# Performance work log

Measured on AMD Instinct MI355X. Metric: run time of the kernel, lower is better.

## Reference

```python
import math
import jax, jax.numpy as jnp
import numpy as np

WQ = (24, 24)  # query window size
WK = (12, 12)  # key window size
NH = 8         # heads
D = 256        # d_model


def _ln(x, g, b, eps=1e-5):
    m = x.mean(-1, keepdims=True)
    v = ((x - m) ** 2).mean(-1, keepdims=True)
    return (x - m) / jnp.sqrt(v + eps) * g + b


def _sine_pos(F, Hp, Wp):
    # Faithful to PositionEmbeddingSine(normalize=True) applied to an NHWC tensor:
    # dim F (grid height) plays the role of channels; returns (F, Hp, Wp).
    npf = F // 2
    scale = 2.0 * math.pi
    eps = 1e-5
    y = jnp.arange(1, Hp + 1, dtype=jnp.float32) / (Hp + eps) * scale
    x = jnp.arange(1, Wp + 1, dtype=jnp.float32) / (Wp + eps) * scale
    dim_t = 10000.0 ** (2.0 * (jnp.arange(npf) // 2).astype(jnp.float32) / npf)
    def enc(e):
        p = e[:, None] / dim_t
        return jnp.stack([jnp.sin(p[:, 0::2]), jnp.cos(p[:, 1::2])], axis=2).reshape(e.shape[0], npf)
    py = enc(y)  # (Hp, npf)
    px = enc(x)  # (Wp, npf)
    pos = jnp.concatenate([
        jnp.broadcast_to(py[:, None, :], (Hp, Wp, npf)),
        jnp.broadcast_to(px[None, :, :], (Hp, Wp, npf))], axis=-1)
    return pos.transpose(2, 0, 1)


def _interp_ac(x, Ho, Wo):
    # bilinear, align_corners=True; x: (B, C, H, W)
    B, C, H, W = x.shape
    ys = jnp.linspace(0.0, H - 1.0, Ho)
    xs = jnp.linspace(0.0, W - 1.0, Wo)
    y0 = jnp.floor(ys).astype(jnp.int32); y1 = jnp.minimum(y0 + 1, H - 1); wy = ys - y0
    x0 = jnp.floor(xs).astype(jnp.int32); x1 = jnp.minimum(x0 + 1, W - 1); wx = xs - x0
    rows = x[:, :, y0, :] * (1 - wy)[None, None, :, None] + x[:, :, y1, :] * wy[None, None, :, None]
    return rows[:, :, :, x0] * (1 - wx) + rows[:, :, :, x1] * wx


def _wpart(x, wh, ww):
    B, H, W, C = x.shape
    return x.reshape(B, H // wh, wh, W // ww, ww, C).transpose(0, 1, 3, 2, 4, 5).reshape(-1, wh * ww, C)


def _avgpool(x, wh, ww):
    B, H, W, C = x.shape
    return x.reshape(B, H // wh, wh, W // ww, ww, C).mean(axis=(2, 4))


def _forward(x1, x2, q_w, q_b, k_w, k_b, v_w, v_b, q2_w, q2_b, k2_w, k2_b, v2_w, v2_b,
             proj_w, proj_b, proj_g, proj_beta, n1_g, n1_b, n2_g, n2_b,
             fc1_w, fc1_b, fc2_w, fc2_b):
    B, C1, H1, W1 = x1.shape
    _, C2, H2, W2 = x2.shape
    hd = D // NH
    x1n = x1.transpose(0, 2, 3, 1)
    sc = _ln(x1n @ proj_w + proj_b, proj_g, proj_beta)
    sc = _interp_ac(sc.transpose(0, 3, 1, 2), H2, W2).transpose(0, 2, 3, 1)
    x1p = jnp.pad(x1n, ((0, 0), (0, (-H1) % WK[0]), (0, (-W1) % WK[1]), (0, 0)))
    x2n = x2.transpose(0, 2, 3, 1)
    x2p = jnp.pad(x2n, ((0, 0), (0, (-H2) % WQ[0]), (0, (-W2) % WQ[1]), (0, 0)))
    H2p, W2p = x2p.shape[1], x2p.shape[2]
    qw = _wpart(x2p, *WQ)  # (B*nw, 576, C2)
    kw = _wpart(x1p, *WK)  # (B*nw, 144, C1)
    Bn, N1, _ = qw.shape
    def heads(t):
        return t.reshape(t.shape[0], t.shape[1], NH, hd).transpose(0, 2, 1, 3)
    q = heads(qw @ q_w + q_b)
    k = heads(kw @ k_w + k_b)
    v = heads(kw @ v_w + v_b)
    # NOTE: faithful to the source: scale = head_dim**(-0.0) == 1.0 and NO softmax here
    attn = q @ k.transpose(0, 1, 3, 2)
    o = (attn @ v).transpose(0, 2, 1, 3).reshape(Bn, N1, D)
    nwh, nww = H2p // WQ[0], W2p // WQ[1]
    o = o.reshape(B, nwh, nww, WQ[0], WQ[1], D).transpose(0, 1, 3, 2, 4, 5).reshape(B, H2p, W2p, D)
    qf = x2p + o
    # global (pooled) cross-attention branch
    qg = _avgpool(x2p, *WQ)
    qg = qg + _sine_pos(qg.shape[1], qg.shape[2], qg.shape[3])[None]
    kg = _avgpool(x1p, *WK)
    kg = kg + _sine_pos(kg.shape[1], kg.shape[2], kg.shape[3])[None]
    qg = qg.reshape(B, -1, C2)
    kg = kg.reshape(B, -1, C1)
    Nw = qg.shape[1]
    qg2 = heads(qg @ q2_w + q2_b)
    kg2 = heads(kg @ k2_w + k2_b)
    vg = heads(kg @ v2_w + v2_b)
    a2 = jax.nn.softmax(qg2 @ kg2.transpose(0, 1, 3, 2), axis=-1)
    og = (a2 @ vg).transpose(0, 2, 1, 3).reshape(B, Nw, D)
    og = og.transpose(0, 2, 1).reshape(B, D, nwh, nww)
    og = _interp_ac(og, H2p, W2p).transpose(0, 2, 3, 1)
    qf = (qf + og)[:, :H2, :W2, :]
    h = _ln(qf, n1_g, n1_b)
    h = jax.nn.gelu(h @ fc1_w + fc1_b, approximate=False) @ fc2_w + fc2_b
    out = sc + h
    return _ln(out, n2_g, n2_b).transpose(0, 3, 1, 2)


def setup_inputs() -> dict:
    key = jax.random.key(0)
    ks = jax.random.split(key, 12)
    B, C1, C2 = 2, 512, 256
    H1, W1, H2, W2 = 96, 96, 192, 192
    s = 0.02
    def lin(k, i, o):
        return jax.random.normal(k, (i, o), jnp.float32) * s
    return {
        'x1': jax.random.normal(ks[0], (B, C1, H1, W1), jnp.float32),
        'x2': jax.random.normal(ks[1], (B, C2, H2, W2), jnp.float32),
        'q_w': lin(ks[2], C2, D), 'q_b': jnp.zeros((D,), jnp.float32),
        'k_w': lin(ks[3], C1, D), 'k_b': jnp.zeros((D,), jnp.float32),
        'v_w': lin(ks[4], C1, D), 'v_b': jnp.zeros((D,), jnp.float32),
        'q2_w': lin(ks[5], C2, D), 'q2_b': jnp.zeros((D,), jnp.float32),
        'k2_w': lin(ks[6], C1, D), 'k2_b': jnp.zeros((D,), jnp.float32),
        'v2_w': lin(ks[7], C1, D), 'v2_b': jnp.zeros((D,), jnp.float32),
        'proj_w': lin(ks[8], C1, D), 'proj_b': jnp.zeros((D,), jnp.float32),
        'proj_g': jnp.ones((D,), jnp.float32), 'proj_beta': jnp.zeros((D,), jnp.float32),
        'n1_g': jnp.ones((D,), jnp.float32), 'n1_b': jnp.zeros((D,), jnp.float32),
        'n2_g': jnp.ones((D,), jnp.float32), 'n2_b': jnp.zeros((D,), jnp.float32),
        'fc1_w': lin(ks[9], D, 2 * D), 'fc1_b': jnp.zeros((2 * D,), jnp.float32),
        'fc2_w': lin(ks[10], 2 * D, D), 'fc2_b': jnp.zeros((D,), jnp.float32),
    }


def reference(x1, x2, q_w, q_b, k_w, k_b, v_w, v_b, q2_w, q2_b, k2_w, k2_b, v2_w, v2_b,
              proj_w, proj_b, proj_g, proj_beta, n1_g, n1_b, n2_g, n2_b,
              fc1_w, fc1_b, fc2_w, fc2_b):
    return _forward(x1, x2, q_w, q_b, k_w, k_b, v_w, v_b, q2_w, q2_b, k2_w, k2_b, v2_w, v2_b,
                    proj_w, proj_b, proj_g, proj_beta, n1_g, n1_b, n2_g, n2_b,
                    fc1_w, fc1_b, fc2_w, fc2_b)
```

## Files before the change

kernel.cpp:

```cpp
#include <hip/hip_runtime.h>
#include <math.h>


#define HW1 9216L
#define HW2 36864L
#define M1  18432L
#define M2  73728L

typedef __attribute__((ext_vector_type(8))) short short8;
typedef __attribute__((ext_vector_type(4))) float f32x4;
typedef unsigned short u16;

__device__ __forceinline__ short f2bf(float f)
{
    unsigned u = __builtin_bit_cast(unsigned, f);
    u = (u + 0x7fff + ((u >> 16) & 1)) >> 16;
    return (short)u;
}
__device__ __forceinline__ float bf2f(u16 u)
{
    unsigned x = ((unsigned)u) << 16;
    return __builtin_bit_cast(float, x);
}
__device__ __forceinline__ float gelu_exact(float v)
{
    return 0.5f * v * (1.0f + erff(v * 0.70710678118654752f));
}

__global__ __launch_bounds__(256) void wcvt(
    const float* __restrict__ pw, const float* __restrict__ kw,
    const float* __restrict__ vw, const float* __restrict__ qw,
    const float* __restrict__ f1, const float* __restrict__ f2,
    u16* __restrict__ pwT, u16* __restrict__ kwT, u16* __restrict__ vwT,
    u16* __restrict__ qwT, u16* __restrict__ f1T, u16* __restrict__ f2T)
{
    int bx = blockIdx.x, t = threadIdx.x;
    const float* src; u16* dst; int K, ldN = 256, kt, n0 = 0;
    if (bx < 32)       { src = pw; dst = pwT; K = 512; kt = bx; }
    else if (bx < 64)  { src = kw; dst = kwT; K = 512; kt = bx - 32; }
    else if (bx < 96)  { src = vw; dst = vwT; K = 512; kt = bx - 64; }
    else if (bx < 112) { src = qw; dst = qwT; K = 256; kt = bx - 96; }
    else if (bx < 144) { int j = bx - 112; src = f1; dst = f1T; K = 256;
                         ldN = 512; kt = j >> 1; n0 = (j & 1) * 256; }
    else               { src = f2; dst = f2T; K = 512; kt = bx - 144; }
    int n = n0 + t, k0 = kt * 16;
    short s[16];
#pragma unroll
    for (int kk = 0; kk < 16; ++kk) s[kk] = f2bf(src[(long)(k0 + kk) * ldN + n]);
    *(short8*)&dst[(long)n * K + k0]     = *(short8*)&s[0];
    *(short8*)&dst[(long)n * K + k0 + 8] = *(short8*)&s[8];
}

__device__ __forceinline__ float pe4(int t, float e)
{
    if (t == 0) return sinf(e);
    if (t == 1) return cosf(e);
    if (t == 2) return sinf(e * 0.01f);
    return cosf(e * 0.01f);
}

__global__ __launch_bounds__(256) void x1t(
    const float* __restrict__ x1, u16* __restrict__ x1bf, float* __restrict__ kg)
{
    __shared__ short T[6144];
    __shared__ float rw[64][8];
    const int blk = blockIdx.x;
    const int b = blk / 768, rem = blk % 768;
    const int cg = rem / 96, y = rem % 96;
    const int t = threadIdx.x;

    ((float2*)rw)[t] = float2{0.f, 0.f};
    __syncthreads();

    const float* src = x1 + ((long)(b * 512 + cg * 64)) * HW1 + (long)y * 96;
#pragma unroll
    for (int k = 0; k < 6; ++k) {
        int idx = t + k * 256;
        int c = idx / 24, col4 = idx % 24;
        float4 v = *(const float4*)(src + (long)c * HW1 + col4 * 4);
        atomicAdd(&rw[c][col4 / 3], v.x + v.y + v.z + v.w);
        int chh = c >> 1, cb = c & 1;
        const float* vf = (const float*)&v;
#pragma unroll
        for (int j = 0; j < 4; ++j) {
            int pix = col4 * 4 + j;
            int word = pix * 32 + (chh ^ (((pix >> 2) & 7) << 2));
            T[word * 2 + cb] = f2bf(vf[j]);
        }
    }
    __syncthreads();
    u16* dst = x1bf + ((long)b * HW1 + (long)y * 96) * 512 + cg * 64;
#pragma unroll
    for (int k = 0; k < 3; ++k) {
        int idx = t + k * 256;
        int pix = idx >> 3, j = idx & 7;
        int w0 = pix * 32 + ((j * 4) ^ (((pix >> 2) & 7) << 2));
        *(short8*)(dst + (long)pix * 512 + j * 8) = *(short8*)&T[w0 * 2];
    }

    {
        int wy = y / 12;
#pragma unroll
        for (int u = 0; u < 2; ++u) {
            int cell = t * 2 + u;
            int c = cell >> 3, wx = cell & 7;
            atomicAdd(kg + (long)(b * 64 + wy * 8 + wx) * 512 + cg * 64 + c,
                      rw[c][wx] * (1.0f / 144.0f));
        }
    }
    if (y % 12 == 0) {
        const float TWO_PI = 6.283185307179586f;
        int wy = y / 12;
#pragma unroll
        for (int u = 0; u < 2; ++u) {
            int cell = t * 2 + u;
            int gxx = cell & 7, c = cg * 64 + (cell >> 3);
            float pos;
            if (wy < 4) pos = pe4(wy,     (gxx + 1) * (TWO_PI / (8.0f + 1e-5f)));
            else        pos = pe4(wy - 4, (c + 1)   * (TWO_PI / (512.0f + 1e-5f)));
            atomicAdd(kg + (long)(b * 64 + wy * 8 + gxx) * 512 + c, pos);
        }
    }
}

__global__ __launch_bounds__(256) void x2t(
    const float* __restrict__ x2, u16* __restrict__ x2pm, float* __restrict__ qg)
{
    __shared__ short T[12288];
    __shared__ float qsum[64][8];
    const int blk = blockIdx.x;
    const int b = blk / 768, rem = blk % 768;
    const int cg = rem / 192, h = rem % 192;
    const int t = threadIdx.x;

    ((float2*)qsum)[t] = float2{0.f, 0.f};
    __syncthreads();

    const float* src = x2 + ((long)(b * 256 + cg * 64) * 192 + h) * 192;
#pragma unroll
    for (int k = 0; k < 12; ++k) {
        int idx = t + k * 256;
        int c = idx / 48, col4 = idx % 48;
        float4 v = *(const float4*)(src + (long)c * HW2 + col4 * 4);
        atomicAdd(&qsum[c][col4 / 6], v.x + v.y + v.z + v.w);
        int chh = c >> 1, cb = c & 1;
        const float* vf = (const float*)&v;
#pragma unroll
        for (int j = 0; j < 4; ++j) {
            int pix = col4 * 4 + j;
            int word = pix * 32 + (chh ^ (((pix >> 2) & 7) << 2));
            T[word * 2 + cb] = f2bf(vf[j]);
        }
    }
    __syncthreads();

    u16* dst = x2pm + ((long)b * HW2 + (long)h * 192) * 256 + cg * 64;
#pragma unroll
    for (int k = 0; k < 6; ++k) {
        int idx = t + k * 256;
        int pix = idx >> 3, j = idx & 7;
        int w0 = pix * 32 + ((j * 4) ^ (((pix >> 2) & 7) << 2));
        *(short8*)(dst + (long)pix * 256 + j * 8) = *(short8*)&T[w0 * 2];
    }

    {
        int wy = h / 24;
#pragma unroll
        for (int u = 0; u < 2; ++u) {
            int cell = t * 2 + u;
            int c = cell >> 3, wx = cell & 7;
            atomicAdd(qg + (long)(b * 64 + wy * 8 + wx) * 256 + cg * 64 + c,
                      qsum[c][wx] * (1.0f / 576.0f));
        }
    }
    if (h % 24 == 0) {
        const float TWO_PI = 6.283185307179586f;
        int wy = h / 24;
#pragma unroll
        for (int u = 0; u < 2; ++u) {
            int cell = t * 2 + u;
            int gxx = cell & 7, c = cg * 64 + (cell >> 3);
            float pos;
            if (wy < 4) pos = pe4(wy,     (gxx + 1) * (TWO_PI / (8.0f + 1e-5f)));
            else        pos = pe4(wy - 4, (c + 1)   * (TWO_PI / (256.0f + 1e-5f)));
            atomicAdd(qg + (long)(b * 64 + wy * 8 + gxx) * 256 + c, pos);
        }
    }
}

template<int EPI, typename TC>
__global__ __launch_bounds__(256) void gemm_lds(
    const u16* __restrict__ A, const u16* __restrict__ BT,
    const float* __restrict__ bias, TC* __restrict__ C,
    int N, int K, int ldA)
{
    __shared__ short pool[18432];
    short* As = pool;
    short* Bs = pool + 128 * 72;
    const int tid = threadIdx.x;
    const int m0 = blockIdx.y * 128;
    const int n0 = blockIdx.x * 128;
    const int w = tid >> 6, lane = tid & 63;
    const int wm = (w & 1) * 64, wn = (w >> 1) * 64;
    const int lm = lane & 15, lq = lane >> 4;

    const int sr = tid >> 1, sh = (tid & 1) * 32;
    const u16* Ap = A  + (long)(m0 + sr) * ldA + sh;
    const u16* Bp = BT + (long)(n0 + sr) * K   + sh;

    f32x4 acc[4][4] = {};

    for (int k0 = 0; k0 < K; k0 += 64) {
#pragma unroll
        for (int q = 0; q < 4; ++q)
            *(short8*)&As[sr * 72 + sh + q * 8] = *(const short8*)(Ap + k0 + q * 8);
#pragma unroll
        for (int q = 0; q < 4; ++q)
            *(short8*)&Bs[sr * 72 + sh + q * 8] = *(const short8*)(Bp + k0 + q * 8);
        __syncthreads();
#pragma unroll
        for (int kk = 0; kk < 64; kk += 32) {
            short8 af[4], bfr[4];
#pragma unroll
            for (int r = 0; r < 4; ++r) af[r]  = *(short8*)&As[(wm + r * 16 + lm) * 72 + kk + lq * 8];
#pragma unroll
            for (int c = 0; c < 4; ++c) bfr[c] = *(short8*)&Bs[(wn + c * 16 + lm) * 72 + kk + lq * 8];
#pragma unroll
            for (int r = 0; r < 4; ++r)
#pragma unroll
                for (int c = 0; c < 4; ++c)
                    acc[r][c] = __builtin_amdgcn_mfma_f32_16x16x32_bf16(af[r], bfr[c], acc[r][c], 0, 0, 0);
        }
        __syncthreads();
    }

    if constexpr (sizeof(TC) == 4) {
#pragma unroll
        for (int r = 0; r < 4; ++r)
#pragma unroll
            for (int i = 0; i < 4; ++i) {
                long row = (long)(m0 + wm + r * 16 + lq * 4 + i) * N;
#pragma unroll
                for (int c = 0; c < 4; ++c) {
                    int col = n0 + wn + c * 16 + lm;
                    ((float*)C)[row + col] = acc[r][c][i] + bias[col];
                }
            }
    } else {
        short* ob = pool;
#pragma unroll
        for (int r = 0; r < 4; ++r)
#pragma unroll
            for (int i = 0; i < 4; ++i) {
                int row = wm + r * 16 + lq * 4 + i;
#pragma unroll
                for (int c = 0; c < 4; ++c) {
                    int jl = wn + c * 16 + lm;
                    float v = acc[r][c][i] + bias[n0 + jl];
                    if (EPI == 1) v = gelu_exact(v);
                    ob[row * 136 + jl] = f2bf(v);
                }
            }
        __syncthreads();
        int m = tid >> 1, half = (tid & 1) * 64;
        u16* Cp = (u16*)C + (long)(m0 + m) * N + n0 + half;
#pragma unroll
        for (int q = 0; q < 8; ++q)
            *(short8*)(Cp + q * 8) = *(short8*)&ob[m * 136 + half + q * 8];
    }
}

__global__ __launch_bounds__(256) void wattn_ln2(
    const u16* __restrict__ x2pm, const u16* __restrict__ qwbT,
    const float* __restrict__ qbias, const u16* __restrict__ ktvb,
    const float* __restrict__ og, u16* __restrict__ hln,
    const float* __restrict__ n1g, const float* __restrict__ n1b)
{
    __shared__ short qs[48 * 288];

    const int t = threadIdx.x;
    const int blk = blockIdx.x;
    const int strip = blk % 12, win = blk / 12;
    const int b = win >> 6, wy = (win >> 3) & 7, wxw = win & 7;
    const int hh0 = wy * 24 + strip * 2;
    const int w = t >> 6, lane = t & 63;
    const int lm = lane & 15, lq = lane >> 4;

    long pbase[3];
#pragma unroll
    for (int r = 0; r < 3; ++r) {
        int p = r * 16 + lm;
        pbase[r] = ((long)b * HW2 + (long)(hh0 + p / 24) * 192 + wxw * 24 + (p % 24)) * 256;
    }

    f32x4 acc[3][4] = {};
#pragma unroll 2
    for (int kc = 0; kc < 8; ++kc) {
        const int ko = kc * 32 + lq * 8;
        short8 af[3], bfr[4];
#pragma unroll
        for (int r = 0; r < 3; ++r)
            af[r] = *(const short8*)(x2pm + pbase[r] + ko);
#pragma unroll
        for (int c = 0; c < 4; ++c)
            bfr[c] = *(const short8*)(qwbT + (long)(w * 64 + c * 16 + lm) * 256 + ko);
#pragma unroll
        for (int r = 0; r < 3; ++r)
#pragma unroll
            for (int c = 0; c < 4; ++c)
                acc[r][c] = __builtin_amdgcn_mfma_f32_16x16x32_bf16(af[r], bfr[c], acc[r][c], 0, 0, 0);
    }

#pragma unroll
    for (int c = 0; c < 4; ++c) {
        float bv = qbias[w * 64 + c * 16 + lm];
#pragma unroll
        for (int r = 0; r < 3; ++r)
#pragma unroll
            for (int i = 0; i < 4; ++i) {
                int row = r * 16 + lq * 4 + i;
                int col = w * 64 + c * 16 + lm;
                qs[row * 288 + (col ^ (((row >> 2) & 3) << 3))] = f2bf(acc[r][c][i] + bv);
            }
    }

    f32x4 oacc[2][3][2] = {};
#pragma unroll
    for (int hl = 0; hl < 2; ++hl) {
        int h = w * 2 + hl;
        short8 af2[3], bfr2[2];
#pragma unroll
        for (int r = 0; r < 3; ++r) {
            int row = r * 16 + lm;
            af2[r] = *(short8*)&qs[row * 288 + ((h * 32 + lq * 8) ^ (((row >> 2) & 3) << 3))];
        }
#pragma unroll
        for (int c = 0; c < 2; ++c)
            bfr2[c] = *(const short8*)(ktvb + ((long)(win * 8 + h) * 32 + c * 16 + lm) * 32 + lq * 8);
#pragma unroll
        for (int r = 0; r < 3; ++r)
#pragma unroll
            for (int c = 0; c < 2; ++c)
                oacc[hl][r][c] = __builtin_amdgcn_mfma_f32_16x16x32_bf16(af2[r], bfr2[c], oacc[hl][r][c], 0, 0, 0);
    }

#pragma unroll
    for (int hl = 0; hl < 2; ++hl)
#pragma unroll
        for (int c = 0; c < 2; ++c)
#pragma unroll
            for (int r = 0; r < 3; ++r)
#pragma unroll
                for (int i = 0; i < 4; ++i) {
                    int p = r * 16 + lq * 4 + i;
                    int ch = (w * 2 + hl) * 32 + c * 16 + lm;
                    qs[p * 288 + (ch ^ (((p >> 2) & 3) << 3))] = f2bf(oacc[hl][r][c][i]);
                }
    __syncthreads();

    float4 g4 = *(const float4*)(n1g + lane * 4);
    float4 b4 = *(const float4*)(n1b + lane * 4);
    const float* ogb0 = og + (long)b * 64 * 256;
#pragma unroll
    for (int pp = 0; pp < 12; ++pp) {
        int p = w * 12 + pp;
        int hh = hh0 + (p / 24), ww = wxw * 24 + (p % 24);
        float fy = hh * (7.0f / 191.0f);
        int y0 = (int)fy; int y1 = min(y0 + 1, 7); float wyf = fy - y0;
        float fx = ww * (7.0f / 191.0f);
        int x0 = (int)fx; int x1 = min(x0 + 1, 7); float wxf = fx - x0;
        float w00 = (1.f - wyf) * (1.f - wxf), w01 = (1.f - wyf) * wxf;
        float w10 = wyf * (1.f - wxf),         w11 = wyf * wxf;
        float4 q00 = *(const float4*)(ogb0 + (y0 * 8 + x0) * 256 + lane * 4);
        float4 q01 = *(const float4*)(ogb0 + (y0 * 8 + x1) * 256 + lane * 4);
        float4 q10 = *(const float4*)(ogb0 + (y1 * 8 + x0) * 256 + lane * 4);
        float4 q11 = *(const float4*)(ogb0 + (y1 * 8 + x1) * 256 + lane * 4);
        long pix = (long)b * HW2 + (long)hh * 192 + ww;
        ushort4 rv = *(const ushort4*)(x2pm + pix * 256 + lane * 4);
        int sw = ((p >> 2) & 3) << 3;
        ushort4 ov = *(ushort4*)&qs[p * 288 + ((lane * 4) ^ sw)];
        float xv0 = bf2f(rv.x) + bf2f(ov.x) + (w00 * q00.x + w01 * q01.x + w10 * q10.x + w11 * q11.x);
        float xv1 = bf2f(rv.y) + bf2f(ov.y) + (w00 * q00.y + w01 * q01.y + w10 * q10.y + w11 * q11.y);
        float xv2 = bf2f(rv.z) + bf2f(ov.z) + (w00 * q00.z + w01 * q01.z + w10 * q10.z + w11 * q11.z);
        float xv3 = bf2f(rv.w) + bf2f(ov.w) + (w00 * q00.w + w01 * q01.w + w10 * q10.w + w11 * q11.w);
        float s  = xv0 + xv1 + xv2 + xv3;
        float s2 = xv0 * xv0 + xv1 * xv1 + xv2 * xv2 + xv3 * xv3;
#pragma unroll
        for (int o = 32; o > 0; o >>= 1) {
            s  += __shfl_xor(s,  o, 64);
            s2 += __shfl_xor(s2, o, 64);
        }
        float mean = s * (1.0f / 256.0f);
        float var  = s2 * (1.0f / 256.0f) - mean * mean;
        float rs   = rsqrtf(var + 1e-5f);
        ushort4 o4;
        o4.x = (u16)f2bf((xv0 - mean) * rs * g4.x + b4.x);
        o4.y = (u16)f2bf((xv1 - mean) * rs * g4.y + b4.y);
        o4.z = (u16)f2bf((xv2 - mean) * rs * g4.z + b4.z);
        o4.w = (u16)f2bf((xv3 - mean) * rs * g4.w + b4.w);
        *(ushort4*)(hln + pix * 256 + lane * 4) = o4;
    }
}

__global__ __launch_bounds__(256) void ln_sc(
    const float* __restrict__ in, u16* __restrict__ out,
    const float* __restrict__ g, const float* __restrict__ b)
{
    __shared__ float sb[4];
    long m = blockIdx.x;
    int t = threadIdx.x;
    float x = in[m * 256 + t];
    float v = x;
#pragma unroll
    for (int o = 32; o > 0; o >>= 1) v += __shfl_down(v, o, 64);
    int wv = t >> 6;
    if ((t & 63) == 0) sb[wv] = v;
    __syncthreads();
    float mean = (sb[0] + sb[1] + sb[2] + sb[3]) * (1.0f / 256.0f);
    __syncthreads();
    float d = x - mean;
    float v2 = d * d;
#pragma unroll
    for (int o = 32; o > 0; o >>= 1) v2 += __shfl_down(v2, o, 64);
    if ((t & 63) == 0) sb[wv] = v2;
    __syncthreads();
    float var = (sb[0] + sb[1] + sb[2] + sb[3]) * (1.0f / 256.0f);
    out[m * 256 + t] = (u16)f2bf(d * rsqrtf(var + 1e-5f) * g[t] + b[t]);
}

__global__ __launch_bounds__(256) void ktv_kernel(
    const u16* __restrict__ kb, const u16* __restrict__ vb,
    u16* __restrict__ ktvb)
{
    int blk = blockIdx.x;
    int win = blk >> 3, hd = blk & 7;
    int b = win >> 6, wy = (win >> 3) & 7, wx = win & 7;
    __shared__ float ks[144][33];
    __shared__ float vs[144][33];
    int t = threadIdx.x;
#pragma unroll
    for (int it = 0; it < 18; ++it) {
        int idx = t + it * 256;
        int p = idx >> 5, c = idx & 31;
        int py = p / 12, px = p % 12;
        long m = (long)b * HW1 + (long)(wy * 12 + py) * 96 + wx * 12 + px;
        ks[p][c] = bf2f(kb[m * 256 + hd * 32 + c]);
        vs[p][c] = bf2f(vb[m * 256 + hd * 32 + c]);
    }
    __syncthreads();
    int i = t >> 3, j0 = (t & 7) * 4;
    float acc[4] = {0.f, 0.f, 0.f, 0.f};
    for (int p = 0; p < 144; ++p) {
        float kv = ks[p][i];
#pragma unroll
        for (int jj = 0; jj < 4; ++jj) acc[jj] += kv * vs[p][j0 + jj];
    }
    long ob = (long)blk * 32 * 32;
#pragma unroll
    for (int jj = 0; jj < 4; ++jj)
        ktvb[ob + (j0 + jj) * 32 + i] = (u16)f2bf(acc[jj]);
}

__global__ __launch_bounds__(256) void gemm64m(
    const float* __restrict__ qg, const float* __restrict__ kg,
    const float* __restrict__ q2w, const float* __restrict__ q2b,
    const float* __restrict__ k2w, const float* __restrict__ k2b,
    const float* __restrict__ v2w, const float* __restrict__ v2b,
    float* __restrict__ qg2, float* __restrict__ kg2, float* __restrict__ vgb)
{
    const float* A; const float* Bm; const float* bias; float* C; int K, ldA;
    int z = blockIdx.z;
    if (z == 0)      { A = qg; Bm = q2w; bias = q2b; C = qg2; K = 256; ldA = 256; }
    else if (z == 1) { A = kg; Bm = k2w; bias = k2b; C = kg2; K = 512; ldA = 512; }
    else             { A = kg; Bm = v2w; bias = v2b; C = vgb; K = 512; ldA = 512; }
    const int N = 256;
    constexpr int BK = 16;
    __shared__ float As[BK][68];
    __shared__ float Bs[BK][68];
    const int tid = threadIdx.x;
    const int m0 = blockIdx.y * 64;
    const int n0 = blockIdx.x * 64;
    const int tm = (tid >> 4) << 2;
    const int tn = (tid & 15) << 2;
    float acc[4][4] = {};
    for (int k0 = 0; k0 < K; k0 += BK) {
#pragma unroll
        for (int it = 0; it < 4; ++it) {
            int idx = tid + it * 256;
            int my = idx >> 4, kx = idx & 15;
            As[kx][my] = A[(long)(m0 + my) * ldA + (k0 + kx)];
        }
#pragma unroll
        for (int it = 0; it < 4; ++it) {
            int idx = tid + it * 256;
            int ky = idx >> 6, nx = idx & 63;
            Bs[ky][nx] = Bm[(long)(k0 + ky) * N + (n0 + nx)];
        }
        __syncthreads();
#pragma unroll
        for (int kk = 0; kk < BK; ++kk) {
            float a[4], b[4];
#pragma unroll
            for (int i = 0; i < 4; ++i) a[i] = As[kk][tm + i];
#pragma unroll
            for (int j = 0; j < 4; ++j) b[j] = Bs[kk][tn + j];
#pragma unroll
            for (int i = 0; i < 4; ++i)
#pragma unroll
                for (int j = 0; j < 4; ++j) acc[i][j] += a[i] * b[j];
        }
        __syncthreads();
    }
#pragma unroll
    for (int i = 0; i < 4; ++i) {
        long row = (long)(m0 + tm + i) * N;
#pragma unroll
        for (int j = 0; j < 4; ++j)
            C[row + n0 + tn + j] = acc[i][j] + bias[n0 + tn + j];
    }
}

__global__ __launch_bounds__(256) void gattn(
    const float* __restrict__ qg2, const float* __restrict__ kg2,
    const float* __restrict__ vg, float* __restrict__ og)
{
    __shared__ float qh[64][33], kh[64][33], vh[64][33];
    __shared__ float S[64][65];
    __shared__ float rinv[64];
    int blk = blockIdx.x;
    int b = blk >> 3, hd = blk & 7;
    int t = threadIdx.x;
#pragma unroll
    for (int it = 0; it < 8; ++it) {
        int idx = t + it * 256;
        int n = idx >> 5, i = idx & 31;
        long src = (long)(b * 64 + n) * 256 + hd * 32 + i;
        qh[n][i] = qg2[src];
        kh[n][i] = kg2[src];
        vh[n][i] = vg[src];
    }
    __syncthreads();
    int r = t >> 2, qq = t & 3, c0 = qq * 16;
    for (int c = c0; c < c0 + 16; ++c) {
        float s = 0.f;
#pragma unroll
        for (int i = 0; i < 32; ++i) s += qh[r][i] * kh[c][i];
        S[r][c] = s;
    }
    __syncthreads();
    float mx = -1e30f;
    for (int c = c0; c < c0 + 16; ++c) mx = fmaxf(mx, S[r][c]);
    mx = fmaxf(mx, __shfl_xor(mx, 1, 64));
    mx = fmaxf(mx, __shfl_xor(mx, 2, 64));
    float sm = 0.f;
    for (int c = c0; c < c0 + 16; ++c) {
        float e = expf(S[r][c] - mx);
        S[r][c] = e;
        sm += e;
    }
    sm += __shfl_xor(sm, 1, 64);
    sm += __shfl_xor(sm, 2, 64);
    if (qq == 0) rinv[r] = 1.0f / sm;
    __syncthreads();
    int n = t >> 2, j0 = (t & 3) * 8;
    float inv = rinv[n];
    for (int j = j0; j < j0 + 8; ++j) {
        float s = 0.f;
        for (int c = 0; c < 64; ++c) s += S[n][c] * vh[c][j];
        og[(long)(b * 64 + n) * 256 + hd * 32 + j] = s * inv;
    }
}

__global__ __launch_bounds__(256) void final_k3(
    const u16* __restrict__ mlp, const u16* __restrict__ sc,
    const float* __restrict__ g, const float* __restrict__ bb,
    float* __restrict__ out)
{
    __shared__ float lnb[32][258];
    int blk = blockIdx.x;
    int b = blk / 1152;
    int rem = blk - b * 1152;
    int hh = rem / 6, ww0 = (rem % 6) * 32;
    int wv = threadIdx.x >> 6, lane = threadIdx.x & 63;
    int c0 = lane * 4;
    float4 g4 = *(const float4*)(g + c0);
    float4 b4 = *(const float4*)(bb + c0);
    float fy = hh * (95.0f / 191.0f);
    int y0 = (int)fy; int y1 = min(y0 + 1, 95); float wy = fy - y0;
    const u16* scb = sc + (long)b * 9216 * 256 + c0;
#pragma unroll
    for (int i = 0; i < 8; ++i) {
        int p = wv * 8 + i;
        int ww = ww0 + p;
        float fx = ww * (95.0f / 191.0f);
        int x0 = (int)fx; int x1 = min(x0 + 1, 95); float wx = fx - x0;
        ushort4 u00 = *(const ushort4*)(scb + (long)(y0 * 96 + x0) * 256);
        ushort4 u01 = *(const ushort4*)(scb + (long)(y0 * 96 + x1) * 256);
        ushort4 u10 = *(const ushort4*)(scb + (long)(y1 * 96 + x0) * 256);
        ushort4 u11 = *(const ushort4*)(scb + (long)(y1 * 96 + x1) * 256);
        long m = ((long)b * 192 + hh) * 192 + ww;
        ushort4 um = *(const ushort4*)(mlp + m * 256 + c0);
        float w00 = (1.f - wy) * (1.f - wx), w01 = (1.f - wy) * wx;
        float w10 = wy * (1.f - wx),         w11 = wy * wx;
        float xv0 = bf2f(um.x) + w00 * bf2f(u00.x) + w01 * bf2f(u01.x) + w10 * bf2f(u10.x) + w11 * bf2f(u11.x);
        float xv1 = bf2f(um.y) + w00 * bf2f(u00.y) + w01 * bf2f(u01.y) + w10 * bf2f(u10.y) + w11 * bf2f(u11.y);
        float xv2 = bf2f(um.z) + w00 * bf2f(u00.z) + w01 * bf2f(u01.z) + w10 * bf2f(u10.z) + w11 * bf2f(u11.z);
        float xv3 = bf2f(um.w) + w00 * bf2f(u00.w) + w01 * bf2f(u01.w) + w10 * bf2f(u10.w) + w11 * bf2f(u11.w);
        float s  = xv0 + xv1 + xv2 + xv3;
        float s2 = xv0 * xv0 + xv1 * xv1 + xv2 * xv2 + xv3 * xv3;
#pragma unroll
        for (int o = 32; o > 0; o >>= 1) {
            s  += __shfl_xor(s,  o, 64);
            s2 += __shfl_xor(s2, o, 64);
        }
        float mean = s * (1.0f / 256.0f);
        float var  = s2 * (1.0f / 256.0f) - mean * mean;
        float rs   = rsqrtf(var + 1e-5f);
        lnb[p][c0 + 0] = (xv0 - mean) * rs * g4.x + b4.x;
        lnb[p][c0 + 1] = (xv1 - mean) * rs * g4.y + b4.y;
        lnb[p][c0 + 2] = (xv2 - mean) * rs * g4.z + b4.z;
        lnb[p][c0 + 3] = (xv3 - mean) * rs * g4.w + b4.w;
    }
    __syncthreads();
    int tw = threadIdx.x & 31, cg = threadIdx.x >> 5;
#pragma unroll
    for (int cc = 0; cc < 32; ++cc) {
        int c = cg * 32 + cc;
        out[((long)(b * 256 + c) * 192 + hh) * 192 + ww0 + tw] = lnb[tw][c];
    }
}

extern "C" void kernel_launch(void* const* d_in, const int* in_sizes, int n_in,
                              void* d_out, int out_size, void* d_ws, size_t ws_size,
                              hipStream_t stream)
{
    const float* x1     = (const float*)d_in[0];
    const float* x2     = (const float*)d_in[1];
    const float* q_w    = (const float*)d_in[2];
    const float* q_b    = (const float*)d_in[3];
    const float* k_w    = (const float*)d_in[4];
    const float* k_b    = (const float*)d_in[5];
    const float* v_w    = (const float*)d_in[6];
    const float* v_b    = (const float*)d_in[7];
    const float* q2_w   = (const float*)d_in[8];
    const float* q2_b   = (const float*)d_in[9];
    const float* k2_w   = (const float*)d_in[10];
    const float* k2_b   = (const float*)d_in[11];
    const float* v2_w   = (const float*)d_in[12];
    const float* v2_b   = (const float*)d_in[13];
    const float* proj_w = (const float*)d_in[14];
    const float* proj_b = (const float*)d_in[15];
    const float* proj_g = (const float*)d_in[16];
    const float* proj_bt= (const float*)d_in[17];
    const float* n1_g   = (const float*)d_in[18];
    const float* n1_b   = (const float*)d_in[19];
    const float* n2_g   = (const float*)d_in[20];
    const float* n2_b   = (const float*)d_in[21];
    const float* fc1_w  = (const float*)d_in[22];
    const float* fc1_b  = (const float*)d_in[23];
    const float* fc2_w  = (const float*)d_in[24];
    const float* fc2_b  = (const float*)d_in[25];
    float* out = (float*)d_out;

    char* p = (char*)d_ws;
    float* scf  = (float*)p;  p += M1 * 256 * 4;
    u16*   scb  = (u16*)p;    p += M1 * 256 * 2;
    u16*   ktvb = (u16*)p;
    u16*   qwT  = (u16*)(p + 2097152);
    u16*   pwT  = qwT + 65536;
    u16*   kwT  = pwT + 131072;
    u16*   vwT  = kwT + 131072;
    u16*   f1T  = vwT + 131072;
    u16*   f2T  = f1T + 131072;
    p += 1024L * 32 * 32 * 4;
    u16*   kb16 = (u16*)p;    p += M1 * 256 * 2;
    u16*   vb16 = (u16*)p;    p += M1 * 256 * 2;
    u16*   hln  = (u16*)p;    p += M2 * 256 * 2;
    u16*   h1c  = (u16*)p;    p += 18432L * 512 * 2;
    u16*   mlpb = (u16*)p;    p += M2 * 256 * 2;
    float* qg   = (float*)p;  p += 128L * 256 * 4;
    float* kg   = (float*)p;  p += 128L * 512 * 4;
    float* qg2  = (float*)p;  p += 128L * 256 * 4;
    float* kg2  = (float*)p;  p += 128L * 256 * 4;
    float* vgb  = (float*)p;  p += 128L * 256 * 4;
    float* ogb  = (float*)p;  p += 128L * 256 * 4;

    u16* x2pm = mlpb;
    u16* x1bf = hln;

    dim3 blk(256);

    hipMemsetAsync(qg, 0, (128L * 256 + 128L * 512) * 4, stream);

    wcvt<<<dim3(176), blk, 0, stream>>>(proj_w, k_w, v_w, q_w, fc1_w, fc2_w,
                                        pwT, kwT, vwT, qwT, f1T, f2T);
    x1t<<<dim3(1536), blk, 0, stream>>>(x1, x1bf, kg);
    x2t<<<dim3(1536), blk, 0, stream>>>(x2, x2pm, qg);

    gemm_lds<0, float><<<dim3(2, 144), blk, 0, stream>>>(x1bf, pwT, proj_b, scf, 256, 512, 512);
    ln_sc<<<dim3(18432), blk, 0, stream>>>(scf, scb, proj_g, proj_bt);

    gemm_lds<0, u16><<<dim3(2, 144), blk, 0, stream>>>(x1bf, kwT, k_b, kb16, 256, 512, 512);
    gemm_lds<0, u16><<<dim3(2, 144), blk, 0, stream>>>(x1bf, vwT, v_b, vb16, 256, 512, 512);

    ktv_kernel<<<dim3(1024), blk, 0, stream>>>(kb16, vb16, ktvb);

    gemm64m<<<dim3(4, 2, 3), blk, 0, stream>>>(qg, kg, q2_w, q2_b, k2_w, k2_b,
                                               v2_w, v2_b, qg2, kg2, vgb);
    gattn<<<dim3(16), blk, 0, stream>>>(qg2, kg2, vgb, ogb);

    wattn_ln2<<<dim3(1536), blk, 0, stream>>>(x2pm, qwT, q_b, ktvb, ogb, hln, n1_g, n1_b);

    for (int c4 = 0; c4 < 4; ++c4) {
        const u16* aoff = hln  + (long)c4 * 18432 * 256;
        u16*       coff = mlpb + (long)c4 * 18432 * 256;
        gemm_lds<1, u16><<<dim3(4, 144), blk, 0, stream>>>(aoff, f1T, fc1_b, h1c, 512, 256, 256);
        gemm_lds<0, u16><<<dim3(2, 144), blk, 0, stream>>>(h1c, f2T, fc2_b, coff, 256, 512, 512);
    }

    final_k3<<<dim3(2304), blk, 0, stream>>>(mlpb, scb, n2_g, n2_b, out);
}
```

Measured before the change: 602.9 us.

## Fuse proj GEMM with LayerNorm, fuse MLP fc1/fc2, and use MFMA for K^T V

Three separate changes. The projection GEMM now applies LayerNorm in its epilogue over full 256-wide rows, removing the fp32 intermediate buffer and the separate ln_sc pass. The two MLP GEMMs are fused into one kernel that keeps the GELU hidden chunk in LDS, replacing eight launches and the h1c round trip through memory. Per-window K^T V now runs on 64-thread MFMA blocks with transposed, zero-padded LDS tiles instead of scalar FMA loops; the fused MLP reads weights straight from global memory without LDS staging, which may raise cache traffic.

```diff
diff --git a/kernel.cpp b/kernel.cpp
--- a/kernel.cpp
+++ b/kernel.cpp
@@ -188,10 +188,86 @@
     }
 }
 
-template<int EPI, typename TC>
+__global__ __launch_bounds__(256) void proj_ln(
+    const u16* __restrict__ A, const u16* __restrict__ BT,
+    const float* __restrict__ bias, const float* __restrict__ g,
+    const float* __restrict__ beta, u16* __restrict__ Cout)
+{
+    __shared__ short pool[64 * 72 + 256 * 72];
+    short* As = pool;
+    short* Bs = pool + 64 * 72;
+    const int t = threadIdx.x;
+    const long m0 = (long)blockIdx.x * 64;
+    const int w = t >> 6, lane = t & 63;
+    const int lm = lane & 15, lq = lane >> 4;
+
+    f32x4 acc[16] = {};
+    for (int k0 = 0; k0 < 512; k0 += 64) {
+#pragma unroll
+        for (int it = 0; it < 2; ++it) {
+            int idx = t + it * 256;
+            int r = idx >> 3, q = idx & 7;
+            *(short8*)&As[r * 72 + q * 8] = *(const short8*)(A + (m0 + r) * 512 + k0 + q * 8);
+        }
+#pragma unroll
+        for (int it = 0; it < 8; ++it) {
+            int idx = t + it * 256;
+            int n = idx >> 3, q = idx & 7;
+            *(short8*)&Bs[n * 72 + q * 8] = *(const short8*)(BT + (long)n * 512 + k0 + q * 8);
+        }
+        __syncthreads();
+#pragma unroll
+        for (int kk = 0; kk < 64; kk += 32) {
+            short8 af = *(short8*)&As[(w * 16 + lm) * 72 + kk + lq * 8];
+#pragma unroll
+            for (int c = 0; c < 16; ++c) {
+                short8 bf = *(short8*)&Bs[(c * 16 + lm) * 72 + kk + lq * 8];
+                acc[c] = __builtin_amdgcn_mfma_f32_16x16x32_bf16(af, bf, acc[c], 0, 0, 0);
+            }
+        }
+        __syncthreads();
+    }
+#pragma unroll
+    for (int c = 0; c < 16; ++c) {
+        float bv = bias[c * 16 + lm];
+#pragma unroll
+        for (int i = 0; i < 4; ++i) acc[c][i] += bv;
+    }
+    short* ob = pool;
+#pragma unroll
+    for (int i = 0; i < 4; ++i) {
+        float s = 0.f, s2 = 0.f;
+#pragma unroll
+        for (int c = 0; c < 16; ++c) { float v = acc[c][i]; s += v; s2 += v * v; }
+#pragma unroll
+        for (int o = 8; o > 0; o >>= 1) {
+            s  += __shfl_xor(s,  o, 64);
+            s2 += __shfl_xor(s2, o, 64);
+        }
+        float mean = s * (1.0f / 256.0f);
+        float var  = s2 * (1.0f / 256.0f) - mean * mean;
+        float rs   = rsqrtf(var + 1e-5f);
+        int row = w * 16 + lq * 4 + i;
+#pragma unroll
+        for (int c = 0; c < 16; ++c) {
+            int col = c * 16 + lm;
+            ob[row * 264 + col] = f2bf((acc[c][i] - mean) * rs * g[col] + beta[col]);
+        }
+    }
+    __syncthreads();
+    {
+        int sr = t >> 2, q4 = (t & 3) * 64;
+        u16* Cp = Cout + (m0 + sr) * 256 + q4;
+#pragma unroll
+        for (int q = 0; q < 8; ++q)
+            *(short8*)(Cp + q * 8) = *(short8*)&ob[sr * 264 + q4 + q * 8];
+    }
+}
+
+template<int EPI>
 __global__ __launch_bounds__(256) void gemm_lds(
     const u16* __restrict__ A, const u16* __restrict__ BT,
-    const float* __restrict__ bias, TC* __restrict__ C,
+    const float* __restrict__ bias, u16* __restrict__ C,
     int N, int K, int ldA)
 {
     __shared__ short pool[18432];
@@ -234,39 +310,92 @@
         __syncthreads();
     }
 
-    if constexpr (sizeof(TC) == 4) {
-#pragma unroll
-        for (int r = 0; r < 4; ++r)
-#pragma unroll
-            for (int i = 0; i < 4; ++i) {
-                long row = (long)(m0 + wm + r * 16 + lq * 4 + i) * N;
-#pragma unroll
-                for (int c = 0; c < 4; ++c) {
-                    int col = n0 + wn + c * 16 + lm;
-                    ((float*)C)[row + col] = acc[r][c][i] + bias[col];
-                }
+    short* ob = pool;
+#pragma unroll
+    for (int r = 0; r < 4; ++r)
+#pragma unroll
+        for (int i = 0; i < 4; ++i) {
+            int row = wm + r * 16 + lq * 4 + i;
+#pragma unroll
+            for (int c = 0; c < 4; ++c) {
+                int jl = wn + c * 16 + lm;
+                float v = acc[r][c][i] + bias[n0 + jl];
+                if (EPI == 1) v = gelu_exact(v);
+                ob[row * 136 + jl] = f2bf(v);
             }
-    } else {
-        short* ob = pool;
-#pragma unroll
-        for (int r = 0; r < 4; ++r)
-#pragma unroll
-            for (int i = 0; i < 4; ++i) {
-                int row = wm + r * 16 + lq * 4 + i;
-#pragma unroll
-                for (int c = 0; c < 4; ++c) {
-                    int jl = wn + c * 16 + lm;
-                    float v = acc[r][c][i] + bias[n0 + jl];
-                    if (EPI == 1) v = gelu_exact(v);
-                    ob[row * 136 + jl] = f2bf(v);
-                }
+        }
+    __syncthreads();
+    int m = tid >> 1, half = (tid & 1) * 64;
+    u16* Cp = C + (long)(m0 + m) * N + n0 + half;
+#pragma unroll
+    for (int q = 0; q < 8; ++q)
+        *(short8*)(Cp + q * 8) = *(short8*)&ob[m * 136 + half + q * 8];
+}
+
+__global__ __launch_bounds__(256) void mlp_fused(
+    const u16* __restrict__ A, const u16* __restrict__ f1T, const float* __restrict__ b1,
+    const u16* __restrict__ f2T, const float* __restrict__ b2, u16* __restrict__ C)
+{
+    __shared__ short As[64 * 264];
+    __shared__ short hs[64 * 136];
+    const int t = threadIdx.x;
+    const long m0 = (long)blockIdx.x * 64;
+    const int w = t >> 6, lane = t & 63;
+    const int lm = lane & 15, lq = lane >> 4;
+
+    {
+        int sr = t >> 2, q4 = (t & 3) * 64;
+        const u16* Ap = A + (m0 + sr) * 256 + q4;
+#pragma unroll
+        for (int q = 0; q < 8; ++q)
+            *(short8*)&As[sr * 264 + q4 + q * 8] = *(const short8*)(Ap + q * 8);
+    }
+
+    f32x4 acc2[16] = {};
+#pragma unroll
+    for (int j = 0; j < 4; ++j) {
+        f32x4 acc1[8] = {};
+#pragma unroll 2
+        for (int kk = 0; kk < 256; kk += 32) {
+            short8 af = *(short8*)&As[(w * 16 + lm) * 264 + kk + lq * 8];
+#pragma unroll
+            for (int c = 0; c < 8; ++c) {
+                short8 bf = *(const short8*)(f1T + (j * 128 + c * 16 + lm) * 256 + kk + lq * 8);
+                acc1[c] = __builtin_amdgcn_mfma_f32_16x16x32_bf16(af, bf, acc1[c], 0, 0, 0);
             }
-        __syncthreads();
-        int m = tid >> 1, half = (tid & 1) * 64;
-        u16* Cp = (u16*)C + (long)(m0 + m) * N + n0 + half;
+        }
+#pragma unroll
+        for (int c = 0; c < 8; ++c) {
+            float bv = b1[j * 128 + c * 16 + lm];
+#pragma unroll
+            for (int i = 0; i < 4; ++i)
+                hs[(w * 16 + lq * 4 + i) * 136 + c * 16 + lm] = f2bf(gelu_exact(acc1[c][i] + bv));
+        }
+#pragma unroll 2
+        for (int kk = 0; kk < 128; kk += 32) {
+            short8 af = *(short8*)&hs[(w * 16 + lm) * 136 + kk + lq * 8];
+#pragma unroll
+            for (int c = 0; c < 16; ++c) {
+                short8 bf = *(const short8*)(f2T + (c * 16 + lm) * 512 + j * 128 + kk + lq * 8);
+                acc2[c] = __builtin_amdgcn_mfma_f32_16x16x32_bf16(af, bf, acc2[c], 0, 0, 0);
+            }
+        }
+    }
+    short* ob = As;
+#pragma unroll
+    for (int c = 0; c < 16; ++c) {
+        float bv = b2[c * 16 + lm];
+#pragma unroll
+        for (int i = 0; i < 4; ++i)
+            ob[(w * 16 + lq * 4 + i) * 264 + c * 16 + lm] = f2bf(acc2[c][i] + bv);
+    }
+    __syncthreads();
+    {
+        int sr = t >> 2, q4 = (t & 3) * 64;
+        u16* Cp = C + (m0 + sr) * 256 + q4;
 #pragma unroll
         for (int q = 0; q < 8; ++q)
-            *(short8*)(Cp + q * 8) = *(short8*)&ob[m * 136 + half + q * 8];
+            *(short8*)(Cp + q * 8) = *(short8*)&ob[sr * 264 + q4 + q * 8];
     }
 }
 
@@ -402,63 +531,62 @@
     }
 }
 
-__global__ __launch_bounds__(256) void ln_sc(
-    const float* __restrict__ in, u16* __restrict__ out,
-    const float* __restrict__ g, const float* __restrict__ b)
-{
-    __shared__ float sb[4];
-    long m = blockIdx.x;
-    int t = threadIdx.x;
-    float x = in[m * 256 + t];
-    float v = x;
-#pragma unroll
-    for (int o = 32; o > 0; o >>= 1) v += __shfl_down(v, o, 64);
-    int wv = t >> 6;
-    if ((t & 63) == 0) sb[wv] = v;
-    __syncthreads();
-    float mean = (sb[0] + sb[1] + sb[2] + sb[3]) * (1.0f / 256.0f);
-    __syncthreads();
-    float d = x - mean;
-    float v2 = d * d;
-#pragma unroll
-    for (int o = 32; o > 0; o >>= 1) v2 += __shfl_down(v2, o, 64);
-    if ((t & 63) == 0) sb[wv] = v2;
-    __syncthreads();
-    float var = (sb[0] + sb[1] + sb[2] + sb[3]) * (1.0f / 256.0f);
-    out[m * 256 + t] = (u16)f2bf(d * rsqrtf(var + 1e-5f) * g[t] + b[t]);
-}
-
-__global__ __launch_bounds__(256) void ktv_kernel(
-    const u16* __restrict__ kb, const u16* __restrict__ vb,
-    u16* __restrict__ ktvb)
-{
-    int blk = blockIdx.x;
-    int win = blk >> 3, hd = blk & 7;
-    int b = win >> 6, wy = (win >> 3) & 7, wx = win & 7;
-    __shared__ float ks[144][33];
-    __shared__ float vs[144][33];
-    int t = threadIdx.x;
-#pragma unroll
-    for (int it = 0; it < 18; ++it) {
-        int idx = t + it * 256;
-        int p = idx >> 5, c = idx & 31;
+__global__ __launch_bounds__(64) void ktv_mfma(
+    const u16* __restrict__ kb, const u16* __restrict__ vb, u16* __restrict__ ktvb)
+{
+    __shared__ short kt[32 * 162];
+    __shared__ short vt[32 * 162];
+    const int blk = blockIdx.x;
+    const int win = blk >> 3, hd = blk & 7;
+    const int b = win >> 6, wy = (win >> 3) & 7, wx = win & 7;
+    const int t = threadIdx.x;
+    const int lm = t & 15, lq = t >> 4;
+
+    {
+        int c = t >> 1, p0 = 144 + (t & 1) * 8;
+#pragma unroll
+        for (int j = 0; j < 8; ++j) {
+            kt[c * 162 + p0 + j] = 0;
+            vt[c * 162 + p0 + j] = 0;
+        }
+    }
+    const int pq = t >> 2, c8 = (t & 3) * 8;
+#pragma unroll
+    for (int it = 0; it < 9; ++it) {
+        int p = it * 16 + pq;
         int py = p / 12, px = p % 12;
         long m = (long)b * HW1 + (long)(wy * 12 + py) * 96 + wx * 12 + px;
-        ks[p][c] = bf2f(kb[m * 256 + hd * 32 + c]);
-        vs[p][c] = bf2f(vb[m * 256 + hd * 32 + c]);
-    }
-    __syncthreads();
-    int i = t >> 3, j0 = (t & 7) * 4;
-    float acc[4] = {0.f, 0.f, 0.f, 0.f};
-    for (int p = 0; p < 144; ++p) {
-        float kv = ks[p][i];
-#pragma unroll
-        for (int jj = 0; jj < 4; ++jj) acc[jj] += kv * vs[p][j0 + jj];
-    }
-    long ob = (long)blk * 32 * 32;
-#pragma unroll
-    for (int jj = 0; jj < 4; ++jj)
-        ktvb[ob + (j0 + jj) * 32 + i] = (u16)f2bf(acc[jj]);
+        short8 kvk = *(const short8*)(kb + m * 256 + hd * 32 + c8);
+        short8 kvv = *(const short8*)(vb + m * 256 + hd * 32 + c8);
+#pragma unroll
+        for (int j = 0; j < 8; ++j) {
+            kt[(c8 + j) * 162 + p] = kvk[j];
+            vt[(c8 + j) * 162 + p] = kvv[j];
+        }
+    }
+    __syncthreads();
+    f32x4 acc[2][2] = {};
+#pragma unroll
+    for (int kk = 0; kk < 160; kk += 32) {
+        short8 af[2], bf[2];
+#pragma unroll
+        for (int r = 0; r < 2; ++r) af[r] = *(short8*)&kt[(r * 16 + lm) * 162 + kk + lq * 8];
+#pragma unroll
+        for (int c = 0; c < 2; ++c) bf[c] = *(short8*)&vt[(c * 16 + lm) * 162 + kk + lq * 8];
+#pragma unroll
+        for (int r = 0; r < 2; ++r)
+#pragma unroll
+            for (int c = 0; c < 2; ++c)
+                acc[r][c] = __builtin_amdgcn_mfma_f32_16x16x32_bf16(af[r], bf[c], acc[r][c], 0, 0, 0);
+    }
+    u16* dst = ktvb + (long)blk * 1024;
+#pragma unroll
+    for (int r = 0; r < 2; ++r)
+#pragma unroll
+        for (int c = 0; c < 2; ++c)
+#pragma unroll
+            for (int i = 0; i < 4; ++i)
+                dst[(c * 16 + lm) * 32 + r * 16 + lq * 4 + i] = (u16)f2bf(acc[r][c][i]);
 }
 
 __global__ __launch_bounds__(256) void gemm64m(
@@ -684,6 +812,7 @@
     float* kg2  = (float*)p;  p += 128L * 256 * 4;
     float* vgb  = (float*)p;  p += 128L * 256 * 4;
     float* ogb  = (float*)p;  p += 128L * 256 * 4;
+    (void)scf; (void)h1c;
 
     u16* x2pm = mlpb;
     u16* x1bf = hln;
@@ -697,13 +826,12 @@
     x1t<<<dim3(1536), blk, 0, stream>>>(x1, x1bf, kg);
     x2t<<<dim3(1536), blk, 0, stream>>>(x2, x2pm, qg);
 
-    gemm_lds<0, float><<<dim3(2, 144), blk, 0, stream>>>(x1bf, pwT, proj_b, scf, 256, 512, 512);
-    ln_sc<<<dim3(18432), blk, 0, stream>>>(scf, scb, proj_g, proj_bt);
-
-    gemm_lds<0, u16><<<dim3(2, 144), blk, 0, stream>>>(x1bf, kwT, k_b, kb16, 256, 512, 512);
-    gemm_lds<0, u16><<<dim3(2, 144), blk, 0, stream>>>(x1bf, vwT, v_b, vb16, 256, 512, 512);
-
-    ktv_kernel<<<dim3(1024), blk, 0, stream>>>(kb16, vb16, ktvb);
+    proj_ln<<<dim3(288), blk, 0, stream>>>(x1bf, pwT, proj_b, proj_g, proj_bt, scb);
+
+    gemm_lds<0><<<dim3(2, 144), blk, 0, stream>>>(x1bf, kwT, k_b, kb16, 256, 512, 512);
+    gemm_lds<0><<<dim3(2, 144), blk, 0, stream>>>(x1bf, vwT, v_b, vb16, 256, 512, 512);
+
+    ktv_mfma<<<dim3(1024), dim3(64), 0, stream>>>(kb16, vb16, ktvb);
 
     gemm64m<<<dim3(4, 2, 3), blk, 0, stream>>>(qg, kg, q2_w, q2_b, k2_w, k2_b,
                                                v2_w, v2_b, qg2, kg2, vgb);
@@ -711,12 +839,7 @@
 
     wattn_ln2<<<dim3(1536), blk, 0, stream>>>(x2pm, qwT, q_b, ktvb, ogb, hln, n1_g, n1_b);
 
-    for (int c4 = 0; c4 < 4; ++c4) {
-        const u16* aoff = hln  + (long)c4 * 18432 * 256;
-        u16*       coff = mlpb + (long)c4 * 18432 * 256;
-        gemm_lds<1, u16><<<dim3(4, 144), blk, 0, stream>>>(aoff, f1T, fc1_b, h1c, 512, 256, 256);
-        gemm_lds<0, u16><<<dim3(2, 144), blk, 0, stream>>>(h1c, f2T, fc2_b, coff, 256, 512, 512);
-    }
+    mlp_fused<<<dim3(1152), blk, 0, stream>>>(hln, f1T, fc1_b, f2T, fc2_b, mlpb);
 
     final_k3<<<dim3(2304), blk, 0, stream>>>(mlpb, scb, n2_g, n2_b, out);
 }
```

Measured after the change: 749.8 us. +24.4%, slower.
